# Kernel tuning notes

Hardware: AMD Instinct MI355X
Metric: run time of the kernel (lower is better)

The kernel has to match this reference:

```python
import jax, jax.numpy as jnp
import numpy as np

ENCODER_DIM, DECODER_DIM, ATTN_DIM = 2048, 512, 512
B, P = 128, 196  # batch, num_pixels (14x14)


def setup_inputs() -> dict:
    key = jax.random.key(0)
    ks = jax.random.split(key, 8)
    s_e = 1.0 / np.sqrt(ENCODER_DIM)
    s_d = 1.0 / np.sqrt(DECODER_DIM)
    s_a = 1.0 / np.sqrt(ATTN_DIM)
    return {
        "encoder_out": jax.random.normal(ks[0], (B, P, ENCODER_DIM), jnp.float32),
        "decoder_hidden": jax.random.normal(ks[1], (B, DECODER_DIM), jnp.float32),
        "W_enc": jax.random.uniform(ks[2], (ENCODER_DIM, ATTN_DIM), jnp.float32, -s_e, s_e),
        "b_enc": jax.random.uniform(ks[3], (ATTN_DIM,), jnp.float32, -s_e, s_e),
        "W_dec": jax.random.uniform(ks[4], (DECODER_DIM, ATTN_DIM), jnp.float32, -s_d, s_d),
        "b_dec": jax.random.uniform(ks[5], (ATTN_DIM,), jnp.float32, -s_d, s_d),
        "W_full": jax.random.uniform(ks[6], (ATTN_DIM,), jnp.float32, -s_a, s_a),
        "b_full": jax.random.uniform(ks[7], (), jnp.float32, -s_a, s_a),
    }


def reference(encoder_out, decoder_hidden, W_enc, b_enc, W_dec, b_dec, W_full, b_full):
    # att1: [B, P, A]; att2: [B, A]
    att1 = jnp.einsum("bpe,ea->bpa", encoder_out, W_enc) + b_enc
    att2 = decoder_hidden @ W_dec + b_dec
    # broadcast add + relu + score projection -> [B, P]
    att = jax.nn.relu(att1 + att2[:, None, :]) @ W_full + b_full
    alpha = jax.nn.softmax(att, axis=1)  # over pixels
    # weighted sum over pixels -> [B, E]
    attention_weighted_encoding = jnp.einsum("bpe,bp->be", encoder_out, alpha)
    return (attention_weighted_encoding, alpha)
```

## Files before the change

### kernel.cpp

```cpp
#include <hip/hip_runtime.h>
#include <hip/hip_bf16.h>

#define ENC_DIM 2048
#define DEC_DIM 512
#define ATT_DIM 512
#define BATCH   128
#define NPIX    196
#define NROWS   (BATCH * NPIX)

typedef short bf16x8 __attribute__((ext_vector_type(8)));
typedef float f32x4  __attribute__((ext_vector_type(4)));
typedef unsigned short u16x8 __attribute__((ext_vector_type(8)));

__device__ __forceinline__ unsigned short f2bf(float f) {
    union { float f; unsigned u; } v; v.f = f;
    unsigned r = v.u + 0x7fffu + ((v.u >> 16) & 1u);
    return (unsigned short)(r >> 16);
}

__global__ void k0_transpose(const float* __restrict__ W_enc,
                             unsigned short* __restrict__ Wt) {
    __shared__ float ts[64][65];
    const int a0 = blockIdx.x * 64;
    const int e0 = blockIdx.y * 64;
    const int tx = threadIdx.x & 15;
    const int ty = threadIdx.x >> 4;
    #pragma unroll
    for (int p = 0; p < 4; ++p) {
        const int e = ty + p * 16;
        const float4 v = *(const float4*)&W_enc[(size_t)(e0 + e) * ATT_DIM + a0 + tx * 4];
        ts[e][tx * 4 + 0] = v.x; ts[e][tx * 4 + 1] = v.y;
        ts[e][tx * 4 + 2] = v.z; ts[e][tx * 4 + 3] = v.w;
    }
    __syncthreads();
    #pragma unroll
    for (int p = 0; p < 4; ++p) {
        const int a = ty + p * 16;
        ushort4 u;
        u.x = f2bf(ts[tx * 4 + 0][a]);
        u.y = f2bf(ts[tx * 4 + 1][a]);
        u.z = f2bf(ts[tx * 4 + 2][a]);
        u.w = f2bf(ts[tx * 4 + 3][a]);
        *(ushort4*)&Wt[(size_t)(a0 + a) * ENC_DIM + e0 + tx * 4] = u;
    }
}

__global__ void k1_att2(const float* __restrict__ dh, const float* __restrict__ W_dec,
                        const float* __restrict__ b_dec, const float* __restrict__ b_enc,
                        const float* __restrict__ b_full,
                        float* __restrict__ att2, float* __restrict__ att) {
    __shared__ float dhs[DEC_DIM];
    const int b = blockIdx.x, t = threadIdx.x;
    dhs[t]       = dh[b * DEC_DIM + t];
    dhs[t + 256] = dh[b * DEC_DIM + t + 256];
    __syncthreads();
    float acc0 = 0.f, acc1 = 0.f;
    for (int d = 0; d < DEC_DIM; ++d) {
        const float h = dhs[d];
        acc0 += h * W_dec[d * ATT_DIM + t];
        acc1 += h * W_dec[d * ATT_DIM + t + 256];
    }
    att2[b * ATT_DIM + t]       = acc0 + b_dec[t]       + b_enc[t];
    att2[b * ATT_DIM + t + 256] = acc1 + b_dec[t + 256] + b_enc[t + 256];
    const int gid = b * 256 + t;
    if (gid < NROWS) att[gid] = b_full[0];
}

__launch_bounds__(256, 4)
__global__ void k2_gemm(const float* __restrict__ enc, const unsigned short* __restrict__ Wt,
                        const float* __restrict__ att2, const float* __restrict__ W_full,
                        float* __restrict__ att) {
    __shared__ __align__(16) unsigned short As[64 * 72];
    __shared__ __align__(16) unsigned short Bs[128 * 72];
    __shared__ float att2s[2][128];
    __shared__ float wfs[128];

    const int t    = threadIdx.x;
    const int n0   = blockIdx.x * 128;
    const int row0 = blockIdx.y * 64;
    const int b0   = row0 / NPIX;
    const int rows_left = (b0 + 1) * NPIX - row0;

    if (t < 128) {
        att2s[0][t] = att2[b0 * ATT_DIM + n0 + t];
        att2s[1][t] = (b0 + 1 < BATCH) ? att2[(b0 + 1) * ATT_DIM + n0 + t] : 0.f;
        wfs[t]      = W_full[n0 + t];
    }

    const int w    = t >> 6;
    const int lane = t & 63;
    const int q    = lane >> 4;
    const int cl   = lane & 15;
    const int wm   = (w >> 1) * 32;
    const int wn   = (w & 1) * 64;

    f32x4 acc[2][4] = {};

    const int ar = t >> 3;
    const int ak = (t & 7) * 8;
    const int bn = t >> 2;
    const int bk = (t & 3) * 16;

    const float*          encA = enc + (size_t)(row0 + ar) * ENC_DIM + ak;
    const unsigned short* WtB  = Wt  + (size_t)(n0 + bn)   * ENC_DIM + bk;

    for (int k0 = 0; k0 < ENC_DIM; k0 += 64) {
        __syncthreads();
        #pragma unroll
        for (int p = 0; p < 2; ++p) {
            const float4 v0 = *(const float4*)(encA + (size_t)p * 32 * ENC_DIM + k0);
            const float4 v1 = *(const float4*)(encA + (size_t)p * 32 * ENC_DIM + k0 + 4);
            u16x8 u;
            u[0] = f2bf(v0.x); u[1] = f2bf(v0.y); u[2] = f2bf(v0.z); u[3] = f2bf(v0.w);
            u[4] = f2bf(v1.x); u[5] = f2bf(v1.y); u[6] = f2bf(v1.z); u[7] = f2bf(v1.w);
            *(u16x8*)&As[(ar + p * 32) * 72 + ak] = u;
        }
        #pragma unroll
        for (int p = 0; p < 2; ++p) {
            const uint4 v0 = *(const uint4*)(WtB + (size_t)p * 64 * ENC_DIM + k0);
            const uint4 v1 = *(const uint4*)(WtB + (size_t)p * 64 * ENC_DIM + k0 + 8);
            *(uint4*)&Bs[(bn + p * 64) * 72 + bk]     = v0;
            *(uint4*)&Bs[(bn + p * 64) * 72 + bk + 8] = v1;
        }
        __syncthreads();

        #pragma unroll
        for (int h = 0; h < 2; ++h) {
            bf16x8 af[2], bfr[4];
            #pragma unroll
            for (int i = 0; i < 2; ++i)
                af[i]  = *(const bf16x8*)&As[(wm + i * 16 + cl) * 72 + h * 32 + q * 8];
            #pragma unroll
            for (int i = 0; i < 4; ++i)
                bfr[i] = *(const bf16x8*)&Bs[(wn + i * 16 + cl) * 72 + h * 32 + q * 8];
            #pragma unroll
            for (int mi = 0; mi < 2; ++mi)
                #pragma unroll
                for (int ni = 0; ni < 4; ++ni)
                    acc[mi][ni] = __builtin_amdgcn_mfma_f32_16x16x32_bf16(
                        af[mi], bfr[ni], acc[mi][ni], 0, 0, 0);
        }
    }

    #pragma unroll
    for (int mi = 0; mi < 2; ++mi) {
        float rs[4];
        #pragma unroll
        for (int i = 0; i < 4; ++i) {
            const int lr  = wm + mi * 16 + q * 4 + i;
            const int sel = (lr >= rows_left) ? 1 : 0;
            float sum = 0.f;
            #pragma unroll
            for (int ni = 0; ni < 4; ++ni) {
                const int j = wn + ni * 16 + cl;
                float v = acc[mi][ni][i] + att2s[sel][j];
                v = fmaxf(v, 0.f);
                sum += v * wfs[j];
            }
            rs[i] = sum;
        }
        #pragma unroll
        for (int o = 1; o < 16; o <<= 1) {
            #pragma unroll
            for (int i = 0; i < 4; ++i) rs[i] += __shfl_xor(rs[i], o);
        }
        if (cl == 0) {
            #pragma unroll
            for (int i = 0; i < 4; ++i) {
                const int r = row0 + wm + mi * 16 + q * 4 + i;
                atomicAdd(&att[r], rs[i]);
            }
        }
    }
}

__global__ void k3_softmax(float* __restrict__ att_alpha) {
    __shared__ float red[4];
    const int b = blockIdx.x, t = threadIdx.x;
    const int w = t >> 6, lane = t & 63;
    const float x = (t < NPIX) ? att_alpha[b * NPIX + t] : -INFINITY;
    float m = x;
    #pragma unroll
    for (int o = 32; o >= 1; o >>= 1) m = fmaxf(m, __shfl_xor(m, o));
    if (lane == 0) red[w] = m;
    __syncthreads();
    m = fmaxf(fmaxf(red[0], red[1]), fmaxf(red[2], red[3]));
    const float e = (t < NPIX) ? __expf(x - m) : 0.f;
    float s = e;
    #pragma unroll
    for (int o = 32; o >= 1; o >>= 1) s += __shfl_xor(s, o);
    __syncthreads();
    if (lane == 0) red[w] = s;
    __syncthreads();
    s = red[0] + red[1] + red[2] + red[3];
    if (t < NPIX) att_alpha[b * NPIX + t] = e / s;
}

__global__ void k4_awe(const float* __restrict__ enc, const float* __restrict__ alpha,
                       float* __restrict__ awe) {
    __shared__ float as[NPIX];
    const int b  = blockIdx.y;
    const int t  = threadIdx.x;
    const int e0 = blockIdx.x * 512 + t * 4;
    as[t] = alpha[b * NPIX + t];
    if (t < NPIX - 128) as[t + 128] = alpha[b * NPIX + t + 128];
    __syncthreads();
    const float* base = enc + (size_t)b * NPIX * ENC_DIM + e0;
    f32x4 a[8] = {};
    for (int p = 0; p < 192; p += 8) {
        #pragma unroll
        for (int j = 0; j < 8; ++j) {
            const f32x4 v = *(const f32x4*)(base + (size_t)(p + j) * ENC_DIM);
            a[j] += as[p + j] * v;
        }
    }
    #pragma unroll
    for (int j = 0; j < 4; ++j) {
        const f32x4 v = *(const f32x4*)(base + (size_t)(192 + j) * ENC_DIM);
        a[j] += as[192 + j] * v;
    }
    const f32x4 r = ((a[0] + a[1]) + (a[2] + a[3])) + ((a[4] + a[5]) + (a[6] + a[7]));
    *(f32x4*)&awe[(size_t)b * ENC_DIM + e0] = r;
}

extern "C" void kernel_launch(void* const* d_in, const int* in_sizes, int n_in,
                              void* d_out, int out_size, void* d_ws, size_t ws_size,
                              hipStream_t stream) {
    const float* enc    = (const float*)d_in[0];
    const float* dh     = (const float*)d_in[1];
    const float* W_enc  = (const float*)d_in[2];
    const float* b_enc  = (const float*)d_in[3];
    const float* W_dec  = (const float*)d_in[4];
    const float* b_dec  = (const float*)d_in[5];
    const float* W_full = (const float*)d_in[6];
    const float* b_full = (const float*)d_in[7];

    float* awe   = (float*)d_out;
    float* alpha = awe + BATCH * ENC_DIM;

    unsigned short* Wt   = (unsigned short*)d_ws;
    float*          att2 = (float*)((char*)d_ws + (size_t)ATT_DIM * ENC_DIM * 2);

    k0_transpose<<<dim3(8, 32),  256, 0, stream>>>(W_enc, Wt);
    k1_att2     <<<128,          256, 0, stream>>>(dh, W_dec, b_dec, b_enc, b_full, att2, alpha);
    k2_gemm     <<<dim3(4, 392), 256, 0, stream>>>(enc, Wt, att2, W_full, alpha);
    k3_softmax  <<<128,          256, 0, stream>>>(alpha);
    k4_awe      <<<dim3(4, 128), 128, 0, stream>>>(enc, alpha, awe);
}
```

Baseline: 435.1 us.

## Widen GEMM N-tile to 256, split att2 and pixel-parallel awe with atomics

```diff
diff --git a/kernel.cpp b/kernel.cpp
--- a/kernel.cpp
+++ b/kernel.cpp
@@ -48,95 +48,93 @@
 __global__ void k1_att2(const float* __restrict__ dh, const float* __restrict__ W_dec,
                         const float* __restrict__ b_dec, const float* __restrict__ b_enc,
                         const float* __restrict__ b_full,
-                        float* __restrict__ att2, float* __restrict__ att) {
+                        float* __restrict__ att2, float* __restrict__ att,
+                        float* __restrict__ awe) {
     __shared__ float dhs[DEC_DIM];
-    const int b = blockIdx.x, t = threadIdx.x;
+    const int c = blockIdx.x, b = blockIdx.y, t = threadIdx.x;
+    const f32x4 z = {0.f, 0.f, 0.f, 0.f};
+    *(f32x4*)&awe[(size_t)b * ENC_DIM + c * 1024 + t * 4] = z;
     dhs[t]       = dh[b * DEC_DIM + t];
     dhs[t + 256] = dh[b * DEC_DIM + t + 256];
     __syncthreads();
-    float acc0 = 0.f, acc1 = 0.f;
-    for (int d = 0; d < DEC_DIM; ++d) {
-        const float h = dhs[d];
-        acc0 += h * W_dec[d * ATT_DIM + t];
-        acc1 += h * W_dec[d * ATT_DIM + t + 256];
-    }
-    att2[b * ATT_DIM + t]       = acc0 + b_dec[t]       + b_enc[t];
-    att2[b * ATT_DIM + t + 256] = acc1 + b_dec[t + 256] + b_enc[t + 256];
-    const int gid = b * 256 + t;
+    const int col = c * 256 + t;
+    float acc = 0.f;
+    for (int d = 0; d < DEC_DIM; ++d)
+        acc += dhs[d] * W_dec[d * ATT_DIM + col];
+    att2[b * ATT_DIM + col] = acc + b_dec[col] + b_enc[col];
+    const int gid = (b * 2 + c) * 256 + t;
     if (gid < NROWS) att[gid] = b_full[0];
 }
 
-__launch_bounds__(256, 4)
+__launch_bounds__(256, 3)
 __global__ void k2_gemm(const float* __restrict__ enc, const unsigned short* __restrict__ Wt,
                         const float* __restrict__ att2, const float* __restrict__ W_full,
                         float* __restrict__ att) {
     __shared__ __align__(16) unsigned short As[64 * 72];
-    __shared__ __align__(16) unsigned short Bs[128 * 72];
-    __shared__ float att2s[2][128];
-    __shared__ float wfs[128];
+    __shared__ __align__(16) unsigned short Bs[256 * 72];
+    __shared__ float att2s[2][256];
+    __shared__ float wfs[256];
 
     const int t    = threadIdx.x;
-    const int n0   = blockIdx.x * 128;
+    const int n0   = blockIdx.x * 256;
     const int row0 = blockIdx.y * 64;
     const int b0   = row0 / NPIX;
     const int rows_left = (b0 + 1) * NPIX - row0;
 
-    if (t < 128) {
-        att2s[0][t] = att2[b0 * ATT_DIM + n0 + t];
-        att2s[1][t] = (b0 + 1 < BATCH) ? att2[(b0 + 1) * ATT_DIM + n0 + t] : 0.f;
-        wfs[t]      = W_full[n0 + t];
-    }
+    att2s[0][t] = att2[b0 * ATT_DIM + n0 + t];
+    att2s[1][t] = (b0 + 1 < BATCH) ? att2[(b0 + 1) * ATT_DIM + n0 + t] : 0.f;
+    wfs[t]      = W_full[n0 + t];
 
     const int w    = t >> 6;
     const int lane = t & 63;
     const int q    = lane >> 4;
     const int cl   = lane & 15;
     const int wm   = (w >> 1) * 32;
-    const int wn   = (w & 1) * 64;
-
-    f32x4 acc[2][4] = {};
-
-    const int ar = t >> 3;
-    const int ak = (t & 7) * 8;
-    const int bn = t >> 2;
-    const int bk = (t & 3) * 16;
+    const int wn   = (w & 1) * 128;
+
+    f32x4 acc[2][8] = {};
+
+    const int ar = t >> 2;
+    const int ak = (t & 3) * 16;
 
     const float*          encA = enc + (size_t)(row0 + ar) * ENC_DIM + ak;
-    const unsigned short* WtB  = Wt  + (size_t)(n0 + bn)   * ENC_DIM + bk;
+    const unsigned short* WtB  = Wt  + (size_t)(n0 + t)    * ENC_DIM;
 
     for (int k0 = 0; k0 < ENC_DIM; k0 += 64) {
         __syncthreads();
-        #pragma unroll
-        for (int p = 0; p < 2; ++p) {
-            const float4 v0 = *(const float4*)(encA + (size_t)p * 32 * ENC_DIM + k0);
-            const float4 v1 = *(const float4*)(encA + (size_t)p * 32 * ENC_DIM + k0 + 4);
-            u16x8 u;
-            u[0] = f2bf(v0.x); u[1] = f2bf(v0.y); u[2] = f2bf(v0.z); u[3] = f2bf(v0.w);
-            u[4] = f2bf(v1.x); u[5] = f2bf(v1.y); u[6] = f2bf(v1.z); u[7] = f2bf(v1.w);
-            *(u16x8*)&As[(ar + p * 32) * 72 + ak] = u;
-        }
-        #pragma unroll
-        for (int p = 0; p < 2; ++p) {
-            const uint4 v0 = *(const uint4*)(WtB + (size_t)p * 64 * ENC_DIM + k0);
-            const uint4 v1 = *(const uint4*)(WtB + (size_t)p * 64 * ENC_DIM + k0 + 8);
-            *(uint4*)&Bs[(bn + p * 64) * 72 + bk]     = v0;
-            *(uint4*)&Bs[(bn + p * 64) * 72 + bk + 8] = v1;
+        {
+            const float4 v0 = *(const float4*)(encA + k0);
+            const float4 v1 = *(const float4*)(encA + k0 + 4);
+            const float4 v2 = *(const float4*)(encA + k0 + 8);
+            const float4 v3 = *(const float4*)(encA + k0 + 12);
+            u16x8 ua, ub;
+            ua[0] = f2bf(v0.x); ua[1] = f2bf(v0.y); ua[2] = f2bf(v0.z); ua[3] = f2bf(v0.w);
+            ua[4] = f2bf(v1.x); ua[5] = f2bf(v1.y); ua[6] = f2bf(v1.z); ua[7] = f2bf(v1.w);
+            ub[0] = f2bf(v2.x); ub[1] = f2bf(v2.y); ub[2] = f2bf(v2.z); ub[3] = f2bf(v2.w);
+            ub[4] = f2bf(v3.x); ub[5] = f2bf(v3.y); ub[6] = f2bf(v3.z); ub[7] = f2bf(v3.w);
+            *(u16x8*)&As[ar * 72 + ak]     = ua;
+            *(u16x8*)&As[ar * 72 + ak + 8] = ub;
+        }
+        #pragma unroll
+        for (int j = 0; j < 8; ++j) {
+            const uint4 v = *(const uint4*)(WtB + k0 + j * 8);
+            *(uint4*)&Bs[t * 72 + j * 8] = v;
         }
         __syncthreads();
 
         #pragma unroll
         for (int h = 0; h < 2; ++h) {
-            bf16x8 af[2], bfr[4];
+            bf16x8 af[2], bfr[8];
             #pragma unroll
             for (int i = 0; i < 2; ++i)
                 af[i]  = *(const bf16x8*)&As[(wm + i * 16 + cl) * 72 + h * 32 + q * 8];
             #pragma unroll
-            for (int i = 0; i < 4; ++i)
+            for (int i = 0; i < 8; ++i)
                 bfr[i] = *(const bf16x8*)&Bs[(wn + i * 16 + cl) * 72 + h * 32 + q * 8];
             #pragma unroll
             for (int mi = 0; mi < 2; ++mi)
                 #pragma unroll
-                for (int ni = 0; ni < 4; ++ni)
+                for (int ni = 0; ni < 8; ++ni)
                     acc[mi][ni] = __builtin_amdgcn_mfma_f32_16x16x32_bf16(
                         af[mi], bfr[ni], acc[mi][ni], 0, 0, 0);
         }
@@ -151,7 +149,7 @@
             const int sel = (lr >= rows_left) ? 1 : 0;
             float sum = 0.f;
             #pragma unroll
-            for (int ni = 0; ni < 4; ++ni) {
+            for (int ni = 0; ni < 8; ++ni) {
                 const int j = wn + ni * 16 + cl;
                 float v = acc[mi][ni][i] + att2s[sel][j];
                 v = fmaxf(v, 0.f);
@@ -198,29 +196,34 @@
 
 __global__ void k4_awe(const float* __restrict__ enc, const float* __restrict__ alpha,
                        float* __restrict__ awe) {
-    __shared__ float as[NPIX];
-    const int b  = blockIdx.y;
+    __shared__ float as[98];
+    const int b  = blockIdx.z;
+    const int p0 = blockIdx.y * 98;
     const int t  = threadIdx.x;
     const int e0 = blockIdx.x * 512 + t * 4;
-    as[t] = alpha[b * NPIX + t];
-    if (t < NPIX - 128) as[t + 128] = alpha[b * NPIX + t + 128];
-    __syncthreads();
-    const float* base = enc + (size_t)b * NPIX * ENC_DIM + e0;
+    if (t < 98) as[t] = alpha[b * NPIX + p0 + t];
+    __syncthreads();
+    const float* base = enc + ((size_t)b * NPIX + p0) * ENC_DIM + e0;
     f32x4 a[8] = {};
-    for (int p = 0; p < 192; p += 8) {
+    for (int p = 0; p < 96; p += 8) {
         #pragma unroll
         for (int j = 0; j < 8; ++j) {
             const f32x4 v = *(const f32x4*)(base + (size_t)(p + j) * ENC_DIM);
             a[j] += as[p + j] * v;
         }
     }
-    #pragma unroll
-    for (int j = 0; j < 4; ++j) {
-        const f32x4 v = *(const f32x4*)(base + (size_t)(192 + j) * ENC_DIM);
-        a[j] += as[192 + j] * v;
+    {
+        const f32x4 v0 = *(const f32x4*)(base + (size_t)96 * ENC_DIM);
+        const f32x4 v1 = *(const f32x4*)(base + (size_t)97 * ENC_DIM);
+        a[0] += as[96] * v0;
+        a[1] += as[97] * v1;
     }
     const f32x4 r = ((a[0] + a[1]) + (a[2] + a[3])) + ((a[4] + a[5]) + (a[6] + a[7]));
-    *(f32x4*)&awe[(size_t)b * ENC_DIM + e0] = r;
+    float* dst = &awe[(size_t)b * ENC_DIM + e0];
+    atomicAdd(dst + 0, r[0]);
+    atomicAdd(dst + 1, r[1]);
+    atomicAdd(dst + 2, r[2]);
+    atomicAdd(dst + 3, r[3]);
 }
 
 extern "C" void kernel_launch(void* const* d_in, const int* in_sizes, int n_in,
@@ -241,9 +244,9 @@
     unsigned short* Wt   = (unsigned short*)d_ws;
     float*          att2 = (float*)((char*)d_ws + (size_t)ATT_DIM * ENC_DIM * 2);
 
-    k0_transpose<<<dim3(8, 32),  256, 0, stream>>>(W_enc, Wt);
-    k1_att2     <<<128,          256, 0, stream>>>(dh, W_dec, b_dec, b_enc, b_full, att2, alpha);
-    k2_gemm     <<<dim3(4, 392), 256, 0, stream>>>(enc, Wt, att2, W_full, alpha);
-    k3_softmax  <<<128,          256, 0, stream>>>(alpha);
-    k4_awe      <<<dim3(4, 128), 128, 0, stream>>>(enc, alpha, awe);
-}
+    k0_transpose<<<dim3(8, 32),     256, 0, stream>>>(W_enc, Wt);
+    k1_att2     <<<dim3(2, 128),    256, 0, stream>>>(dh, W_dec, b_dec, b_enc, b_full, att2, alpha, awe);
+    k2_gemm     <<<dim3(2, 392),    256, 0, stream>>>(enc, Wt, att2, W_full, alpha);
+    k3_softmax  <<<128,             256, 0, stream>>>(alpha);
+    k4_awe      <<<dim3(4, 2, 128), 128, 0, stream>>>(enc, alpha, awe);
+}
```

Measured after the change: 493.9 us. 13.5% more time.
